# Optimization experiments

Hardware: AMD Instinct MI355X
Metric: run time of the kernel (lower is better)

Reference implementation:

```python
import jax, jax.numpy as jnp
import numpy as np

N, E, G = 50000, 800000, 200
F_IN, C, HEADS = 16, 64, 4
HID = C * HEADS  # 256


def setup_inputs() -> dict:
    key = jax.random.key(0)
    ks = jax.random.split(key, 30)
    rn = lambda k, s, sc=0.1: jax.random.normal(k, s, jnp.float32) * sc
    inp = {
        'x': jax.random.normal(ks[0], (N, F_IN), jnp.float32),
        'edge_index': jax.random.randint(ks[1], (2, E), 0, N, jnp.int32),
        'batch': jnp.sort(jax.random.randint(ks[2], (N,), 0, G, jnp.int32)),
        'Wl1': rn(ks[3], (F_IN, HID)), 'Wr1': rn(ks[4], (F_IN, HID)),
        'att1': rn(ks[5], (HEADS, C)), 'b1': rn(ks[6], (HID,)),
        'g1': jnp.ones((HID,), jnp.float32), 'be1': jnp.zeros((HID,), jnp.float32),
        'Wl2': rn(ks[7], (HID, HID)), 'Wr2': rn(ks[8], (HID, HID)),
        'att2': rn(ks[9], (HEADS, C)), 'b2': rn(ks[10], (HID,)),
        'g2': jnp.ones((HID,), jnp.float32), 'be2': jnp.zeros((HID,), jnp.float32),
        # GATv2 layer 3: 256 -> 64, 1 head, mean (concat=False)
        'Wl3': rn(ks[11], (HID, C)), 'Wr3': rn(ks[12], (HID, C)),
        'att3': rn(ks[13], (1, C)), 'b3': rn(ks[14], (C,)),
        'g3': jnp.ones((C,), jnp.float32), 'be3': jnp.zeros((C,), jnp.float32),
        # classifier MLP: 128 -> 64 -> 1
        'Wc1': rn(ks[15], (2 * C, C)), 'bc1': rn(ks[16], (C,)),
        'Wc2': rn(ks[17], (C, 1)), 'bc2': rn(ks[18], (1,)),
    }
    return inp


def _gatv2(x, src, dst, Wl, Wr, att, b, heads, c, concat):
    n = x.shape[0]
    xl = (x @ Wl).reshape(n, heads, c)
    xr = (x @ Wr).reshape(n, heads, c)
    s = jax.nn.leaky_relu(xl[src] + xr[dst], 0.2)       # [E', H, C]
    e = jnp.einsum('ehc,hc->eh', s, att)                 # [E', H]
    m = jax.ops.segment_max(e, dst, num_segments=n)
    p = jnp.exp(e - m[dst])
    denom = jax.ops.segment_sum(p, dst, num_segments=n)
    alpha = p / (denom[dst] + 1e-16)
    out = jax.ops.segment_sum(alpha[:, :, None] * xl[src], dst, num_segments=n)
    out = out.reshape(n, heads * c) if concat else out.mean(axis=1)
    return out + b


def _bn(x, g, b):
    mu = x.mean(0)
    v = x.var(0)
    return (x - mu) * jax.lax.rsqrt(v + 1e-5) * g + b


def reference(x, edge_index, batch,
              Wl1, Wr1, att1, b1, g1, be1,
              Wl2, Wr2, att2, b2, g2, be2,
              Wl3, Wr3, att3, b3, g3, be3,
              Wc1, bc1, Wc2, bc2):
    n = x.shape[0]
    loop = jnp.arange(n, dtype=edge_index.dtype)
    src = jnp.concatenate([edge_index[0], loop])  # PyG add_self_loops=True
    dst = jnp.concatenate([edge_index[1], loop])

    h = _gatv2(x, src, dst, Wl1, Wr1, att1, b1, HEADS, C, True)
    h = jax.nn.elu(_bn(h, g1, be1))  # dropout disabled (eval)
    h = _gatv2(h, src, dst, Wl2, Wr2, att2, b2, HEADS, C, True)
    h = jax.nn.elu(_bn(h, g2, be2))
    h = _gatv2(h, src, dst, Wl3, Wr3, att3, b3, 1, C, False)
    h = _bn(h, g3, be3)

    cnt = jax.ops.segment_sum(jnp.ones((n, 1), h.dtype), batch, num_segments=G)
    mean_pool = jax.ops.segment_sum(h, batch, num_segments=G) / jnp.maximum(cnt, 1.0)
    max_pool = jax.ops.segment_max(h, batch, num_segments=G)
    pooled = jnp.concatenate([mean_pool, max_pool], axis=1)  # [G, 128]

    out = jax.nn.relu(pooled @ Wc1 + bc1)
    out = out @ Wc2 + bc2  # [G, 1]
    return out
```

## Files before the change

### kernel.cpp

```cpp
#include <hip/hip_runtime.h>
#include <math.h>

#define N_NODES 50000
#define N_EDGES 800000
#define ET (N_EDGES + N_NODES)
#define N_GRAPHS 200
#define F_INN 16
#define C_DIM 64
#define N_HEADS 4
#define HIDD 256
#define SCAN_BLOCKS ((N_NODES + 255) / 256)

typedef __attribute__((ext_vector_type(8))) short short8;
typedef __attribute__((ext_vector_type(4))) float f32x4;
typedef __attribute__((ext_vector_type(2))) float f32x2;

__device__ __forceinline__ float bf2f(ushort u) {
  return __uint_as_float(((unsigned)u) << 16);
}
__device__ __forceinline__ ushort f2bf(float f) {
  unsigned u = __float_as_uint(f);
  u += 0x7fff + ((u >> 16) & 1);
  return (ushort)(u >> 16);
}

__device__ __forceinline__ f32x2 emax2(f32x2 a, f32x2 b) {
#if __has_builtin(__builtin_elementwise_max)
  return __builtin_elementwise_max(a, b);
#else
  f32x2 r;
  r.x = fmaxf(a.x, b.x);
  r.y = fmaxf(a.y, b.y);
  return r;
#endif
}

template<int K, int M>
__global__ __launch_bounds__(256) void gemm_dual(
    const float* __restrict__ A, const float* __restrict__ Bl,
    const float* __restrict__ Br, ushort* __restrict__ Clb,
    float* __restrict__ Cr, int nrows)
{
  __shared__ __align__(16) float As[16][64];
  __shared__ __align__(16) float Bls[16][64];
  __shared__ __align__(16) float Brs[16][64];
  int tid = threadIdx.x;
  int row0 = blockIdx.x * 64;
  int col0 = blockIdx.y * 64;
  int tr = (tid >> 4) << 2;
  int tc = (tid & 15) << 2;
  float accL[4][4] = {{0.f}}, accR[4][4] = {{0.f}};
  int arow = tid >> 2, ak = (tid & 3) << 2;
  int brow = tid >> 4, bcol = (tid & 15) << 2;
  for (int k0 = 0; k0 < K; k0 += 16) {
    float4 av = make_float4(0.f, 0.f, 0.f, 0.f);
    int gr = row0 + arow;
    if (gr < nrows) av = *(const float4*)&A[(size_t)gr * K + k0 + ak];
    As[ak + 0][arow] = av.x;
    As[ak + 1][arow] = av.y;
    As[ak + 2][arow] = av.z;
    As[ak + 3][arow] = av.w;
    *(float4*)&Bls[brow][bcol] = *(const float4*)&Bl[(size_t)(k0 + brow) * M + col0 + bcol];
    *(float4*)&Brs[brow][bcol] = *(const float4*)&Br[(size_t)(k0 + brow) * M + col0 + bcol];
    __syncthreads();
    #pragma unroll
    for (int k = 0; k < 16; ++k) {
      float4 a = *(const float4*)&As[k][tr];
      float4 bl = *(const float4*)&Bls[k][tc];
      float4 br = *(const float4*)&Brs[k][tc];
      float aa[4] = {a.x, a.y, a.z, a.w};
      float lb[4] = {bl.x, bl.y, bl.z, bl.w};
      float rb[4] = {br.x, br.y, br.z, br.w};
      #pragma unroll
      for (int ii = 0; ii < 4; ++ii)
        #pragma unroll
        for (int jj = 0; jj < 4; ++jj) {
          accL[ii][jj] = fmaf(aa[ii], lb[jj], accL[ii][jj]);
          accR[ii][jj] = fmaf(aa[ii], rb[jj], accR[ii][jj]);
        }
    }
    __syncthreads();
  }
  #pragma unroll
  for (int ii = 0; ii < 4; ++ii) {
    int gr = row0 + tr + ii;
    if (gr < nrows) {
      *(ushort4*)&Clb[(size_t)gr * M + col0 + tc] =
          make_ushort4(f2bf(accL[ii][0]), f2bf(accL[ii][1]),
                       f2bf(accL[ii][2]), f2bf(accL[ii][3]));
      *(float4*)&Cr[(size_t)gr * M + col0 + tc] =
          make_float4(accR[ii][0], accR[ii][1], accR[ii][2], accR[ii][3]);
    }
  }
}

__device__ __forceinline__ void split_bf16(float a, ushort& hi, ushort& lo) {
  unsigned u = __float_as_uint(a);
  hi = (ushort)(u >> 16);
  float ah = __uint_as_float(u & 0xffff0000u);
  float r = a - ah;
  lo = (ushort)(__float_as_uint(r) >> 16);
}

template<int K, int N>
__global__ void convertB(const float* __restrict__ W, ushort* __restrict__ BTmat) {
  int idx = blockIdx.x * blockDim.x + threadIdx.x;
  if (idx >= K * N) return;
  int k = idx / N, n = idx - k * N;
  ushort hi, lo;
  split_bf16(W[idx], hi, lo);
  size_t dst = ((size_t)(k >> 3) * N + n) * 8 + (k & 7);
  BTmat[dst] = hi;
  BTmat[(size_t)(K / 8) * N * 8 + dst] = lo;
}

template<int N>
__global__ __launch_bounds__(N * 2) void gemm_fused(
    const float* __restrict__ H, const float* __restrict__ gsum,
    const float* __restrict__ gsumsq, const float* __restrict__ g,
    const float* __restrict__ be, const ushort* __restrict__ BT,
    ushort* __restrict__ Clb, float* __restrict__ Cr)
{
  constexpr int THREADS = N * 2;
  constexpr int PLANE = 32 * N * 8;
  __shared__ float SCs[256], SHs[256];
  __shared__ ushort Ah_s[64 * 256];
  __shared__ ushort Al_s[64 * 256];
  const int tid = threadIdx.x;
  const int brow0 = blockIdx.x * 64;

  const float invn = 1.0f / (float)N_NODES;
  for (int c = tid; c < 256; c += THREADS) {
    float mu = gsum[c] * invn;
    float var = gsumsq[c] * invn - mu * mu;
    float sc = g[c] * rsqrtf(var + 1e-5f);
    SCs[c] = sc;
    SHs[c] = be[c] - mu * sc;
  }
  __syncthreads();

  for (int gid = tid; gid < 2048; gid += THREADS) {
    int r = gid >> 5;
    int ch0 = (gid & 31) * 8;
    int grow = min(brow0 + r, N_NODES - 1);
    float4 v0 = *(const float4*)&H[(size_t)grow * 256 + ch0];
    float4 v1 = *(const float4*)&H[(size_t)grow * 256 + ch0 + 4];
    float4 sc0 = *(const float4*)&SCs[ch0];
    float4 sc1 = *(const float4*)&SCs[ch0 + 4];
    float4 sh0 = *(const float4*)&SHs[ch0];
    float4 sh1 = *(const float4*)&SHs[ch0 + 4];
    float vv[8] = {v0.x, v0.y, v0.z, v0.w, v1.x, v1.y, v1.z, v1.w};
    float scv[8] = {sc0.x, sc0.y, sc0.z, sc0.w, sc1.x, sc1.y, sc1.z, sc1.w};
    float shv[8] = {sh0.x, sh0.y, sh0.z, sh0.w, sh1.x, sh1.y, sh1.z, sh1.w};
    short8 hi8, lo8;
    #pragma unroll
    for (int j = 0; j < 8; ++j) {
      float t = fmaf(vv[j], scv[j], shv[j]);
      float e = t > 0.f ? t : __expf(t) - 1.f;
      ushort h, l;
      split_bf16(e, h, l);
      hi8[j] = (short)h;
      lo8[j] = (short)l;
    }
    int off = r * 512 + ((ch0 * 2) ^ ((r & 7) << 4));
    *(short8*)((char*)Ah_s + off) = hi8;
    *(short8*)((char*)Al_s + off) = lo8;
  }
  __syncthreads();

  const int wave = tid >> 6, lane = tid & 63;
  const int cn = lane & 15, kgrp = lane >> 4;
  const int combc = wave * 64;
  const bool isR = combc >= N;
  const ushort* Bh = BT + (isR ? 2 * PLANE : 0);
  const ushort* Bl_ = Bh + PLANE;
  const int cb = combc & (N - 1);
  f32x4 acc[4][4];
  #pragma unroll
  for (int rt = 0; rt < 4; ++rt)
    #pragma unroll
    for (int ct = 0; ct < 4; ++ct) acc[rt][ct] = (f32x4)(0.f);

  #pragma unroll 2
  for (int k0 = 0; k0 < 256; k0 += 32) {
    short8 ah[4], al[4];
    #pragma unroll
    for (int rt = 0; rt < 4; ++rt) {
      int row = rt * 16 + cn;
      int off = row * 512 + (((k0 * 2) + kgrp * 16) ^ ((row & 7) << 4));
      ah[rt] = *(const short8*)((const char*)Ah_s + off);
      al[rt] = *(const short8*)((const char*)Al_s + off);
    }
    const size_t bbase = (size_t)((k0 >> 3) + kgrp) * (N * 8);
    #pragma unroll
    for (int ct = 0; ct < 4; ++ct) {
      const size_t bo = bbase + (size_t)(cb + ct * 16 + cn) * 8;
      short8 bh = *(const short8*)&Bh[bo];
      short8 bl = *(const short8*)&Bl_[bo];
      #pragma unroll
      for (int rt = 0; rt < 4; ++rt) {
        acc[rt][ct] = __builtin_amdgcn_mfma_f32_16x16x32_bf16(ah[rt], bh, acc[rt][ct], 0, 0, 0);
        acc[rt][ct] = __builtin_amdgcn_mfma_f32_16x16x32_bf16(ah[rt], bl, acc[rt][ct], 0, 0, 0);
        acc[rt][ct] = __builtin_amdgcn_mfma_f32_16x16x32_bf16(al[rt], bh, acc[rt][ct], 0, 0, 0);
      }
    }
  }

  #pragma unroll
  for (int ct = 0; ct < 4; ++ct) {
    int cc = cb + ct * 16 + cn;
    #pragma unroll
    for (int rt = 0; rt < 4; ++rt) {
      int crow0 = brow0 + rt * 16 + kgrp * 4;
      #pragma unroll
      for (int j = 0; j < 4; ++j) {
        int rr = crow0 + j;
        if (rr < N_NODES) {
          if (!isR) Clb[(size_t)rr * N + cc] = f2bf(acc[rt][ct][j]);
          else      Cr[(size_t)rr * N + cc] = acc[rt][ct][j];
        }
      }
    }
  }
}

__global__ void hist_kernel(const int* __restrict__ dsts, int* __restrict__ curs) {
  int i = blockIdx.x * blockDim.x + threadIdx.x;
  if (i >= ET) return;
  int d = (i < N_EDGES) ? dsts[i] : i - N_EDGES;
  atomicAdd(&curs[d], 1);
}

__global__ __launch_bounds__(256) void scan_part(
    const int* __restrict__ curs, int* __restrict__ rows, int* __restrict__ bsum)
{
  __shared__ int tmp[256];
  int t = threadIdx.x;
  int i = blockIdx.x * 256 + t;
  int v = (i < N_NODES) ? curs[i] : 0;
  tmp[t] = v;
  __syncthreads();
  #pragma unroll
  for (int off = 1; off < 256; off <<= 1) {
    int u = (t >= off) ? tmp[t - off] : 0;
    __syncthreads();
    tmp[t] += u;
    __syncthreads();
  }
  if (i < N_NODES) rows[i] = tmp[t] - v;
  if (t == 255) bsum[blockIdx.x] = tmp[255];
}

__global__ __launch_bounds__(256) void scan_bsums(
    const int* __restrict__ bsum, int* __restrict__ boff)
{
  __shared__ int tmp[256];
  int t = threadIdx.x;
  int v = (t < SCAN_BLOCKS) ? bsum[t] : 0;
  tmp[t] = v;
  __syncthreads();
  #pragma unroll
  for (int off = 1; off < 256; off <<= 1) {
    int u = (t >= off) ? tmp[t - off] : 0;
    __syncthreads();
    tmp[t] += u;
    __syncthreads();
  }
  if (t < SCAN_BLOCKS) boff[t] = tmp[t] - v;
}

__global__ __launch_bounds__(256) void scan_apply(
    int* __restrict__ rows, const int* __restrict__ boff, int* __restrict__ curs)
{
  int i = blockIdx.x * 256 + threadIdx.x;
  if (i < N_NODES) {
    int r = rows[i] + boff[blockIdx.x];
    rows[i] = r;
    curs[i] = r;
  }
  if (i == 0) rows[N_NODES] = ET;
}

__global__ void scatter_kernel(const int* __restrict__ srcs, const int* __restrict__ dsts,
                               int* __restrict__ curs, int* __restrict__ esrc) {
  int i = blockIdx.x * blockDim.x + threadIdx.x;
  if (i >= ET) return;
  int s, d;
  if (i < N_EDGES) { s = srcs[i]; d = dsts[i]; } else { s = d = i - N_EDGES; }
  int pos = atomicAdd(&curs[d], 1);
  esrc[pos] = s;
}

template<int HEADS_, int D_>
__global__ __launch_bounds__(256) void flash_csr(
    const ushort* __restrict__ xl, const float* __restrict__ xr,
    const float* __restrict__ att, const int* __restrict__ rows,
    const int* __restrict__ esrc, float* __restrict__ out)
{
  int d = blockIdx.x * 4 + (threadIdx.x >> 6);
  if (d >= N_NODES) return;
  int lane = threadIdx.x & 63;
  int beg = rows[d], end = rows[d + 1];
  if constexpr (D_ == 256) {
    float4 xrvf = *(const float4*)&xr[(size_t)d * 256 + lane * 4];
    float4 wf = *(const float4*)&att[lane * 4];
    f32x2 xr01 = {xrvf.x, xrvf.y}, xr23 = {xrvf.z, xrvf.w};
    f32x2 w01 = {wf.x, wf.y}, w23 = {wf.z, wf.w};
    float m = -INFINITY, s = 0.f;
    f32x2 a01 = {0.f, 0.f}, a23 = {0.f, 0.f};

    auto loadb = [&](int src, f32x2& ba, f32x2& bb) {
      ushort4 u = *(const ushort4*)&xl[(size_t)src * 256 + lane * 4];
      ba = f32x2{bf2f(u.x), bf2f(u.y)};
      bb = f32x2{bf2f(u.z), bf2f(u.w)};
    };
    auto scoreP = [&](f32x2 ba, f32x2 bb) -> float {
      f32x2 v01 = ba + xr01, v23 = bb + xr23;
      v01 = emax2(v01, v01 * 0.2f);
      v23 = emax2(v23, v23 * 0.2f);
      f32x2 dd = v01 * w01 + v23 * w23;
      return dd.x + dd.y;
    };
    auto one_edge = [&](int src) {
      f32x2 ba, bb;
      loadb(src, ba, bb);
      float e = scoreP(ba, bb);
      e += __shfl_xor(e, 1);
      e += __shfl_xor(e, 2);
      e += __shfl_xor(e, 4);
      e += __shfl_xor(e, 8);
      float mn = fmaxf(m, e);
      float f = __expf(m - mn);
      float pe = __expf(e - mn);
      s = s * f + pe;
      a01 = a01 * f + ba * pe;
      a23 = a23 * f + bb * pe;
      m = mn;
    };

    int p = beg;
    int head = min(end, (beg + 3) & ~3);
    for (; p < head; ++p) one_edge(esrc[p]);
    for (; p + 4 <= end; p += 4) {
      int4 sv = *(const int4*)&esrc[p];
      f32x2 b1a, b1b, b2a, b2b, b3a, b3b, b4a, b4b;
      loadb(sv.x, b1a, b1b);
      loadb(sv.y, b2a, b2b);
      loadb(sv.z, b3a, b3b);
      loadb(sv.w, b4a, b4b);
      float e1 = scoreP(b1a, b1b);
      float e2 = scoreP(b2a, b2b);
      float e3 = scoreP(b3a, b3b);
      float e4 = scoreP(b4a, b4b);
      e1 += __shfl_xor(e1, 1); e2 += __shfl_xor(e2, 1);
      e3 += __shfl_xor(e3, 1); e4 += __shfl_xor(e4, 1);
      e1 += __shfl_xor(e1, 2); e2 += __shfl_xor(e2, 2);
      e3 += __shfl_xor(e3, 2); e4 += __shfl_xor(e4, 2);
      e1 += __shfl_xor(e1, 4); e2 += __shfl_xor(e2, 4);
      e3 += __shfl_xor(e3, 4); e4 += __shfl_xor(e4, 4);
      e1 += __shfl_xor(e1, 8); e2 += __shfl_xor(e2, 8);
      e3 += __shfl_xor(e3, 8); e4 += __shfl_xor(e4, 8);
      float mn = fmaxf(fmaxf(m, fmaxf(e1, e2)), fmaxf(e3, e4));
      float f = __expf(m - mn);
      float p1 = __expf(e1 - mn);
      float p2 = __expf(e2 - mn);
      float p3 = __expf(e3 - mn);
      float p4 = __expf(e4 - mn);
      s = s * f + ((p1 + p2) + (p3 + p4));
      f32x2 t01 = b1a * p1 + b2a * p2;
      f32x2 u01 = b3a * p3 + b4a * p4;
      a01 = a01 * f + (t01 + u01);
      f32x2 t23 = b1b * p1 + b2b * p2;
      f32x2 u23 = b3b * p3 + b4b * p4;
      a23 = a23 * f + (t23 + u23);
      m = mn;
    }
    for (; p < end; ++p) one_edge(esrc[p]);

    float inv = 1.f / (s + 1e-16f);
    *(float4*)&out[(size_t)d * 256 + lane * 4] =
        make_float4(a01.x * inv, a01.y * inv, a23.x * inv, a23.y * inv);
  } else {
    float xrv = xr[(size_t)d * 64 + lane];
    float w = att[lane];
    float m = -INFINITY, s = 0.f, acc = 0.f;
    int p = beg;
    for (; p + 2 <= end; p += 2) {
      int s1 = esrc[p], s2 = esrc[p + 1];
      float b1 = bf2f(xl[(size_t)s1 * 64 + lane]);
      float b2 = bf2f(xl[(size_t)s2 * 64 + lane]);
      float v1 = b1 + xrv, v2 = b2 + xrv;
      v1 = fmaxf(v1, 0.2f * v1);
      v2 = fmaxf(v2, 0.2f * v2);
      float e1 = v1 * w, e2 = v2 * w;
      e1 += __shfl_xor(e1, 1);  e2 += __shfl_xor(e2, 1);
      e1 += __shfl_xor(e1, 2);  e2 += __shfl_xor(e2, 2);
      e1 += __shfl_xor(e1, 4);  e2 += __shfl_xor(e2, 4);
      e1 += __shfl_xor(e1, 8);  e2 += __shfl_xor(e2, 8);
      e1 += __shfl_xor(e1, 16); e2 += __shfl_xor(e2, 16);
      e1 += __shfl_xor(e1, 32); e2 += __shfl_xor(e2, 32);
      float mn = fmaxf(m, fmaxf(e1, e2));
      float f = __expf(m - mn);
      float p1 = __expf(e1 - mn);
      float p2 = __expf(e2 - mn);
      s = fmaf(s, f, p1 + p2);
      acc = fmaf(acc, f, fmaf(p1, b1, p2 * b2));
      m = mn;
    }
    if (p < end) {
      int s1 = esrc[p];
      float b1 = bf2f(xl[(size_t)s1 * 64 + lane]);
      float v1 = b1 + xrv;
      v1 = fmaxf(v1, 0.2f * v1);
      float e1 = v1 * w;
      e1 += __shfl_xor(e1, 1);
      e1 += __shfl_xor(e1, 2);
      e1 += __shfl_xor(e1, 4);
      e1 += __shfl_xor(e1, 8);
      e1 += __shfl_xor(e1, 16);
      e1 += __shfl_xor(e1, 32);
      float mn = fmaxf(m, e1);
      float f = __expf(m - mn);
      float p1 = __expf(e1 - mn);
      s = fmaf(s, f, p1);
      acc = fmaf(acc, f, p1 * b1);
    }
    out[(size_t)d * 64 + lane] = acc / (s + 1e-16f);
  }
}

template<int D_, int RPB>
__global__ __launch_bounds__(256) void bn_stats(const float* __restrict__ h,
    float* __restrict__ gsum, float* __restrict__ gsumsq, int nrows)
{
  constexpr int RG = 256 / D_;
  int c = threadIdx.x % D_;
  int rg = threadIdx.x / D_;
  int r0 = blockIdx.x * RPB;
  float s = 0.f, sq = 0.f;
  int rend = min(r0 + RPB, nrows);
  for (int r = r0 + rg; r < rend; r += RG) {
    float v = h[(size_t)r * D_ + c];
    s += v;
    sq = fmaf(v, v, sq);
  }
  atomicAdd(&gsum[c], s);
  atomicAdd(&gsumsq[c], sq);
}

__global__ __launch_bounds__(256) void pool_mlp(
    const float* __restrict__ h3, const int* __restrict__ batch,
    const float* __restrict__ gsum, const float* __restrict__ gsumsq,
    const float* __restrict__ g3, const float* __restrict__ be3,
    const float* __restrict__ Wc1, const float* __restrict__ bc1,
    const float* __restrict__ Wc2, const float* __restrict__ bc2,
    float* __restrict__ outp)
{
  int g = blockIdx.x;
  int t = threadIdx.x;
  int lane = t & 63, w = t >> 6;
  int lo, hi;
  {
    int a = 0, b = N_NODES;
    while (a < b) { int mid = (a + b) >> 1; if (batch[mid] < g) a = mid + 1; else b = mid; }
    lo = a;
    b = N_NODES;
    while (a < b) { int mid = (a + b) >> 1; if (batch[mid] < g + 1) a = mid + 1; else b = mid; }
    hi = a;
  }
  const float invn = 1.0f / (float)N_NODES;
  float mu = gsum[lane] * invn;
  float var = gsumsq[lane] * invn - mu * mu;
  float scl = g3[lane] * rsqrtf(var + 1e-5f);
  float shf = be3[lane] - mu * scl;
  float s = 0.f, mx = -INFINITY;
  for (int r = lo + w; r < hi; r += 4) {
    float v = fmaf(h3[(size_t)r * 64 + lane], scl, shf);
    s += v;
    mx = fmaxf(mx, v);
  }
  __shared__ float ssum[4][64];
  __shared__ float smax[4][64];
  __shared__ float pooled[128];
  ssum[w][lane] = s;
  smax[w][lane] = mx;
  __syncthreads();
  if (w == 0) {
    float tot = ssum[0][lane] + ssum[1][lane] + ssum[2][lane] + ssum[3][lane];
    float m4 = fmaxf(fmaxf(smax[0][lane], smax[1][lane]),
                     fmaxf(smax[2][lane], smax[3][lane]));
    float cnt = (float)(hi - lo);
    pooled[lane] = tot / fmaxf(cnt, 1.f);
    pooled[64 + lane] = m4;
  }
  __syncthreads();
  if (w == 0) {
    float a = bc1[lane];
    #pragma unroll 8
    for (int k = 0; k < 128; ++k) a = fmaf(pooled[k], Wc1[k * 64 + lane], a);
    a = fmaxf(a, 0.f);
    float v = a * Wc2[lane];
    v += __shfl_xor(v, 1);
    v += __shfl_xor(v, 2);
    v += __shfl_xor(v, 4);
    v += __shfl_xor(v, 8);
    v += __shfl_xor(v, 16);
    v += __shfl_xor(v, 32);
    if (lane == 0) outp[g] = v + bc2[0];
  }
}

extern "C" void kernel_launch(void* const* d_in, const int* in_sizes, int n_in,
                              void* d_out, int out_size, void* d_ws, size_t ws_size,
                              hipStream_t stream)
{
  const float* x    = (const float*)d_in[0];
  const int*   ei   = (const int*)d_in[1];
  const int*   batch= (const int*)d_in[2];
  const float* Wl1  = (const float*)d_in[3];
  const float* Wr1  = (const float*)d_in[4];
  const float* att1 = (const float*)d_in[5];
  const float* g1   = (const float*)d_in[7];
  const float* be1  = (const float*)d_in[8];
  const float* Wl2  = (const float*)d_in[9];
  const float* Wr2  = (const float*)d_in[10];
  const float* att2 = (const float*)d_in[11];
  const float* g2   = (const float*)d_in[13];
  const float* be2  = (const float*)d_in[14];
  const float* Wl3  = (const float*)d_in[15];
  const float* Wr3  = (const float*)d_in[16];
  const float* att3 = (const float*)d_in[17];
  const float* g3   = (const float*)d_in[19];
  const float* be3  = (const float*)d_in[20];
  const float* Wc1  = (const float*)d_in[21];
  const float* bc1  = (const float*)d_in[22];
  const float* Wc2  = (const float*)d_in[23];
  const float* bc2  = (const float*)d_in[24];

  const int* srcs = ei;
  const int* dsts = ei + N_EDGES;

  float* ws = (float*)d_ws;
  size_t o = 0;
  ushort* XLB = (ushort*)(ws + o); o += (size_t)N_NODES * HIDD / 2;
  float* XR = ws + o;            o += (size_t)N_NODES * HIDD;
  float* Hb = ws + o;            o += (size_t)N_NODES * HIDD;
  ushort* BT2 = (ushort*)(ws + o); o += (size_t)4 * 32 * 256 * 8 / 2;
  ushort* BT3 = (ushort*)(ws + o); o += (size_t)4 * 32 * 64 * 8 / 2;
  int* ESRC = (int*)(ws + o);    o += ET;
  int* ROWS = (int*)(ws + o);    o += N_NODES + 1;
  int* CURS = (int*)(ws + o);    o += N_NODES;
  int* BSUM = (int*)(ws + o);    o += SCAN_BLOCKS;
  int* BOFF = (int*)(ws + o);    o += SCAN_BLOCKS;
  float* GS  = ws + o;           o += 256;
  float* GSQ = ws + o;           o += 256;

  const int ROW_BLOCKS = (N_NODES + 63) / 64;
  const int DST_BLOCKS = (N_NODES + 3) / 4;
  constexpr int PLANE2 = 32 * 256 * 8;
  constexpr int PLANE3 = 32 * 64 * 8;

  convertB<256, 256><<<(65536 + 255) / 256, 256, 0, stream>>>(Wl2, BT2);
  convertB<256, 256><<<(65536 + 255) / 256, 256, 0, stream>>>(Wr2, BT2 + 2 * PLANE2);
  convertB<256, 64><<<(16384 + 255) / 256, 256, 0, stream>>>(Wl3, BT3);
  convertB<256, 64><<<(16384 + 255) / 256, 256, 0, stream>>>(Wr3, BT3 + 2 * PLANE3);

  hipMemsetAsync(CURS, 0, N_NODES * 4, stream);
  hist_kernel<<<(ET + 255) / 256, 256, 0, stream>>>(dsts, CURS);
  scan_part<<<SCAN_BLOCKS, 256, 0, stream>>>(CURS, ROWS, BSUM);
  scan_bsums<<<1, 256, 0, stream>>>(BSUM, BOFF);
  scan_apply<<<SCAN_BLOCKS, 256, 0, stream>>>(ROWS, BOFF, CURS);
  scatter_kernel<<<(ET + 255) / 256, 256, 0, stream>>>(srcs, dsts, CURS, ESRC);

  gemm_dual<16, 256><<<dim3(ROW_BLOCKS, 4), 256, 0, stream>>>(
      x, Wl1, Wr1, XLB, XR, N_NODES);
  flash_csr<4, 256><<<DST_BLOCKS, 256, 0, stream>>>(XLB, XR, att1, ROWS, ESRC, Hb);
  hipMemsetAsync(GS, 0, 512 * 4, stream);
  bn_stats<256, 64><<<ROW_BLOCKS, 256, 0, stream>>>(Hb, GS, GSQ, N_NODES);

  gemm_fused<256><<<ROW_BLOCKS, 512, 0, stream>>>(
      Hb, GS, GSQ, g1, be1, BT2, XLB, XR);
  flash_csr<4, 256><<<DST_BLOCKS, 256, 0, stream>>>(XLB, XR, att2, ROWS, ESRC, Hb);
  hipMemsetAsync(GS, 0, 512 * 4, stream);
  bn_stats<256, 64><<<ROW_BLOCKS, 256, 0, stream>>>(Hb, GS, GSQ, N_NODES);

  gemm_fused<64><<<ROW_BLOCKS, 128, 0, stream>>>(
      Hb, GS, GSQ, g2, be2, BT3, XLB, XR);
  flash_csr<1, 64><<<DST_BLOCKS, 256, 0, stream>>>(XLB, XR, att3, ROWS, ESRC, Hb);
  hipMemsetAsync(GS, 0, 512 * 4, stream);
  bn_stats<64, 256><<<(N_NODES + 255) / 256, 256, 0, stream>>>(Hb, GS, GSQ, N_NODES);

  pool_mlp<<<N_GRAPHS, 256, 0, stream>>>(Hb, batch, GS, GSQ, g3, be3,
                                         Wc1, bc1, Wc2, bc2, (float*)d_out);
}
```

Measured before the change: 604.9 us.

## Pack multiple destination nodes per wavefront in GATv2 aggregation kernels

Result: faster. 577.8 us (-4.5%).

```diff
diff --git a/kernel.cpp b/kernel.cpp
--- a/kernel.cpp
+++ b/kernel.cpp
@@ -12,6 +12,7 @@
 #define SCAN_BLOCKS ((N_NODES + 255) / 256)
 
 typedef __attribute__((ext_vector_type(8))) short short8;
+typedef __attribute__((ext_vector_type(8))) ushort ushort8;
 typedef __attribute__((ext_vector_type(4))) float f32x4;
 typedef __attribute__((ext_vector_type(2))) float f32x2;
 
@@ -291,141 +292,197 @@
   esrc[pos] = s;
 }
 
-template<int HEADS_, int D_>
-__global__ __launch_bounds__(256) void flash_csr(
+__global__ __launch_bounds__(256) void flash256(
     const ushort* __restrict__ xl, const float* __restrict__ xr,
     const float* __restrict__ att, const int* __restrict__ rows,
     const int* __restrict__ esrc, float* __restrict__ out)
 {
-  int d = blockIdx.x * 4 + (threadIdx.x >> 6);
-  if (d >= N_NODES) return;
-  int lane = threadIdx.x & 63;
+  const int wave = threadIdx.x >> 6, lane = threadIdx.x & 63;
+  const int half = lane >> 5, sl = lane & 31;
+  const int d = blockIdx.x * 8 + wave * 2 + half;
+  const int ch = sl * 8;
+  float4 xa = *(const float4*)&xr[(size_t)d * 256 + ch];
+  float4 xb = *(const float4*)&xr[(size_t)d * 256 + ch + 4];
+  float4 wa = *(const float4*)&att[ch];
+  float4 wb = *(const float4*)&att[ch + 4];
+  f32x2 xr0 = {xa.x, xa.y}, xr1 = {xa.z, xa.w}, xr2 = {xb.x, xb.y}, xr3 = {xb.z, xb.w};
+  f32x2 w0 = {wa.x, wa.y}, w1 = {wa.z, wa.w}, w2 = {wb.x, wb.y}, w3 = {wb.z, wb.w};
   int beg = rows[d], end = rows[d + 1];
-  if constexpr (D_ == 256) {
-    float4 xrvf = *(const float4*)&xr[(size_t)d * 256 + lane * 4];
-    float4 wf = *(const float4*)&att[lane * 4];
-    f32x2 xr01 = {xrvf.x, xrvf.y}, xr23 = {xrvf.z, xrvf.w};
-    f32x2 w01 = {wf.x, wf.y}, w23 = {wf.z, wf.w};
-    float m = -INFINITY, s = 0.f;
-    f32x2 a01 = {0.f, 0.f}, a23 = {0.f, 0.f};
-
-    auto loadb = [&](int src, f32x2& ba, f32x2& bb) {
-      ushort4 u = *(const ushort4*)&xl[(size_t)src * 256 + lane * 4];
-      ba = f32x2{bf2f(u.x), bf2f(u.y)};
-      bb = f32x2{bf2f(u.z), bf2f(u.w)};
-    };
-    auto scoreP = [&](f32x2 ba, f32x2 bb) -> float {
-      f32x2 v01 = ba + xr01, v23 = bb + xr23;
-      v01 = emax2(v01, v01 * 0.2f);
-      v23 = emax2(v23, v23 * 0.2f);
-      f32x2 dd = v01 * w01 + v23 * w23;
-      return dd.x + dd.y;
-    };
-    auto one_edge = [&](int src) {
-      f32x2 ba, bb;
-      loadb(src, ba, bb);
-      float e = scoreP(ba, bb);
-      e += __shfl_xor(e, 1);
-      e += __shfl_xor(e, 2);
-      e += __shfl_xor(e, 4);
-      e += __shfl_xor(e, 8);
-      float mn = fmaxf(m, e);
-      float f = __expf(m - mn);
-      float pe = __expf(e - mn);
-      s = s * f + pe;
-      a01 = a01 * f + ba * pe;
-      a23 = a23 * f + bb * pe;
-      m = mn;
-    };
-
-    int p = beg;
-    int head = min(end, (beg + 3) & ~3);
-    for (; p < head; ++p) one_edge(esrc[p]);
-    for (; p + 4 <= end; p += 4) {
-      int4 sv = *(const int4*)&esrc[p];
-      f32x2 b1a, b1b, b2a, b2b, b3a, b3b, b4a, b4b;
-      loadb(sv.x, b1a, b1b);
-      loadb(sv.y, b2a, b2b);
-      loadb(sv.z, b3a, b3b);
-      loadb(sv.w, b4a, b4b);
-      float e1 = scoreP(b1a, b1b);
-      float e2 = scoreP(b2a, b2b);
-      float e3 = scoreP(b3a, b3b);
-      float e4 = scoreP(b4a, b4b);
-      e1 += __shfl_xor(e1, 1); e2 += __shfl_xor(e2, 1);
-      e3 += __shfl_xor(e3, 1); e4 += __shfl_xor(e4, 1);
-      e1 += __shfl_xor(e1, 2); e2 += __shfl_xor(e2, 2);
-      e3 += __shfl_xor(e3, 2); e4 += __shfl_xor(e4, 2);
-      e1 += __shfl_xor(e1, 4); e2 += __shfl_xor(e2, 4);
-      e3 += __shfl_xor(e3, 4); e4 += __shfl_xor(e4, 4);
-      e1 += __shfl_xor(e1, 8); e2 += __shfl_xor(e2, 8);
-      e3 += __shfl_xor(e3, 8); e4 += __shfl_xor(e4, 8);
-      float mn = fmaxf(fmaxf(m, fmaxf(e1, e2)), fmaxf(e3, e4));
-      float f = __expf(m - mn);
-      float p1 = __expf(e1 - mn);
-      float p2 = __expf(e2 - mn);
-      float p3 = __expf(e3 - mn);
-      float p4 = __expf(e4 - mn);
-      s = s * f + ((p1 + p2) + (p3 + p4));
-      f32x2 t01 = b1a * p1 + b2a * p2;
-      f32x2 u01 = b3a * p3 + b4a * p4;
-      a01 = a01 * f + (t01 + u01);
-      f32x2 t23 = b1b * p1 + b2b * p2;
-      f32x2 u23 = b3b * p3 + b4b * p4;
-      a23 = a23 * f + (t23 + u23);
-      m = mn;
-    }
-    for (; p < end; ++p) one_edge(esrc[p]);
-
+  float m = -INFINITY, s = 0.f;
+  f32x2 a0 = {0.f, 0.f}, a1 = {0.f, 0.f}, a2 = {0.f, 0.f}, a3 = {0.f, 0.f};
+
+  auto loadb = [&](int src, f32x2 b[4]) {
+    ushort8 u = *(const ushort8*)&xl[(size_t)src * 256 + ch];
+    b[0] = f32x2{bf2f(u[0]), bf2f(u[1])};
+    b[1] = f32x2{bf2f(u[2]), bf2f(u[3])};
+    b[2] = f32x2{bf2f(u[4]), bf2f(u[5])};
+    b[3] = f32x2{bf2f(u[6]), bf2f(u[7])};
+  };
+  auto scoreP = [&](const f32x2 b[4]) -> float {
+    f32x2 v0 = b[0] + xr0, v1 = b[1] + xr1, v2 = b[2] + xr2, v3 = b[3] + xr3;
+    v0 = emax2(v0, v0 * 0.2f);
+    v1 = emax2(v1, v1 * 0.2f);
+    v2 = emax2(v2, v2 * 0.2f);
+    v3 = emax2(v3, v3 * 0.2f);
+    f32x2 dd = (v0 * w0 + v1 * w1) + (v2 * w2 + v3 * w3);
+    return dd.x + dd.y;
+  };
+  auto one_edge = [&](int src) {
+    f32x2 b[4];
+    loadb(src, b);
+    float e = scoreP(b);
+    e += __shfl_xor(e, 1);
+    e += __shfl_xor(e, 2);
+    e += __shfl_xor(e, 4);
+    float mn = fmaxf(m, e);
+    float f = __expf(m - mn);
+    float pe = __expf(e - mn);
+    s = s * f + pe;
+    a0 = a0 * f + b[0] * pe;
+    a1 = a1 * f + b[1] * pe;
+    a2 = a2 * f + b[2] * pe;
+    a3 = a3 * f + b[3] * pe;
+    m = mn;
+  };
+
+  int p = beg;
+  int hd = min(end, (beg + 3) & ~3);
+  for (; p < hd; ++p) one_edge(esrc[p]);
+  for (; p + 4 <= end; p += 4) {
+    int4 sv = *(const int4*)&esrc[p];
+    f32x2 b1[4], b2[4], b3[4], b4[4];
+    loadb(sv.x, b1);
+    loadb(sv.y, b2);
+    loadb(sv.z, b3);
+    loadb(sv.w, b4);
+    float e1 = scoreP(b1);
+    float e2 = scoreP(b2);
+    float e3 = scoreP(b3);
+    float e4 = scoreP(b4);
+    e1 += __shfl_xor(e1, 1); e2 += __shfl_xor(e2, 1);
+    e3 += __shfl_xor(e3, 1); e4 += __shfl_xor(e4, 1);
+    e1 += __shfl_xor(e1, 2); e2 += __shfl_xor(e2, 2);
+    e3 += __shfl_xor(e3, 2); e4 += __shfl_xor(e4, 2);
+    e1 += __shfl_xor(e1, 4); e2 += __shfl_xor(e2, 4);
+    e3 += __shfl_xor(e3, 4); e4 += __shfl_xor(e4, 4);
+    float mn = fmaxf(fmaxf(m, fmaxf(e1, e2)), fmaxf(e3, e4));
+    float f = __expf(m - mn);
+    float p1 = __expf(e1 - mn);
+    float p2 = __expf(e2 - mn);
+    float p3 = __expf(e3 - mn);
+    float p4 = __expf(e4 - mn);
+    s = s * f + ((p1 + p2) + (p3 + p4));
+    a0 = a0 * f + ((b1[0] * p1 + b2[0] * p2) + (b3[0] * p3 + b4[0] * p4));
+    a1 = a1 * f + ((b1[1] * p1 + b2[1] * p2) + (b3[1] * p3 + b4[1] * p4));
+    a2 = a2 * f + ((b1[2] * p1 + b2[2] * p2) + (b3[2] * p3 + b4[2] * p4));
+    a3 = a3 * f + ((b1[3] * p1 + b2[3] * p2) + (b3[3] * p3 + b4[3] * p4));
+    m = mn;
+  }
+  for (; p < end; ++p) one_edge(esrc[p]);
+
+  float inv = 1.f / (s + 1e-16f);
+  *(float4*)&out[(size_t)d * 256 + ch] =
+      make_float4(a0.x * inv, a0.y * inv, a1.x * inv, a1.y * inv);
+  *(float4*)&out[(size_t)d * 256 + ch + 4] =
+      make_float4(a2.x * inv, a2.y * inv, a3.x * inv, a3.y * inv);
+}
+
+__global__ __launch_bounds__(256) void flash64(
+    const ushort* __restrict__ xl, const float* __restrict__ xr,
+    const float* __restrict__ att, const int* __restrict__ rows,
+    const int* __restrict__ esrc, float* __restrict__ out)
+{
+  const int wave = threadIdx.x >> 6, lane = threadIdx.x & 63;
+  const int di = lane >> 3, sl = lane & 7;
+  const int d = blockIdx.x * 32 + wave * 8 + di;
+  const bool valid = d < N_NODES;
+  const int dc = valid ? d : N_NODES - 1;
+  const int ch = sl * 8;
+  float4 xa = *(const float4*)&xr[(size_t)dc * 64 + ch];
+  float4 xb = *(const float4*)&xr[(size_t)dc * 64 + ch + 4];
+  float4 wa = *(const float4*)&att[ch];
+  float4 wb = *(const float4*)&att[ch + 4];
+  f32x2 xr0 = {xa.x, xa.y}, xr1 = {xa.z, xa.w}, xr2 = {xb.x, xb.y}, xr3 = {xb.z, xb.w};
+  f32x2 w0 = {wa.x, wa.y}, w1 = {wa.z, wa.w}, w2 = {wb.x, wb.y}, w3 = {wb.z, wb.w};
+  int beg = rows[dc], end = rows[dc + 1];
+  float m = -INFINITY, s = 0.f;
+  f32x2 a0 = {0.f, 0.f}, a1 = {0.f, 0.f}, a2 = {0.f, 0.f}, a3 = {0.f, 0.f};
+
+  auto loadb = [&](int src, f32x2 b[4]) {
+    ushort8 u = *(const ushort8*)&xl[(size_t)src * 64 + ch];
+    b[0] = f32x2{bf2f(u[0]), bf2f(u[1])};
+    b[1] = f32x2{bf2f(u[2]), bf2f(u[3])};
+    b[2] = f32x2{bf2f(u[4]), bf2f(u[5])};
+    b[3] = f32x2{bf2f(u[6]), bf2f(u[7])};
+  };
+  auto scoreP = [&](const f32x2 b[4]) -> float {
+    f32x2 v0 = b[0] + xr0, v1 = b[1] + xr1, v2 = b[2] + xr2, v3 = b[3] + xr3;
+    v0 = emax2(v0, v0 * 0.2f);
+    v1 = emax2(v1, v1 * 0.2f);
+    v2 = emax2(v2, v2 * 0.2f);
+    v3 = emax2(v3, v3 * 0.2f);
+    f32x2 dd = (v0 * w0 + v1 * w1) + (v2 * w2 + v3 * w3);
+    return dd.x + dd.y;
+  };
+  auto one_edge = [&](int src) {
+    f32x2 b[4];
+    loadb(src, b);
+    float e = scoreP(b);
+    e += __shfl_xor(e, 1);
+    e += __shfl_xor(e, 2);
+    e += __shfl_xor(e, 4);
+    float mn = fmaxf(m, e);
+    float f = __expf(m - mn);
+    float pe = __expf(e - mn);
+    s = s * f + pe;
+    a0 = a0 * f + b[0] * pe;
+    a1 = a1 * f + b[1] * pe;
+    a2 = a2 * f + b[2] * pe;
+    a3 = a3 * f + b[3] * pe;
+    m = mn;
+  };
+
+  int p = beg;
+  int hd = min(end, (beg + 3) & ~3);
+  for (; p < hd; ++p) one_edge(esrc[p]);
+  for (; p + 4 <= end; p += 4) {
+    int4 sv = *(const int4*)&esrc[p];
+    f32x2 b1[4], b2[4], b3[4], b4[4];
+    loadb(sv.x, b1);
+    loadb(sv.y, b2);
+    loadb(sv.z, b3);
+    loadb(sv.w, b4);
+    float e1 = scoreP(b1);
+    float e2 = scoreP(b2);
+    float e3 = scoreP(b3);
+    float e4 = scoreP(b4);
+    e1 += __shfl_xor(e1, 1); e2 += __shfl_xor(e2, 1);
+    e3 += __shfl_xor(e3, 1); e4 += __shfl_xor(e4, 1);
+    e1 += __shfl_xor(e1, 2); e2 += __shfl_xor(e2, 2);
+    e3 += __shfl_xor(e3, 2); e4 += __shfl_xor(e4, 2);
+    e1 += __shfl_xor(e1, 4); e2 += __shfl_xor(e2, 4);
+    e3 += __shfl_xor(e3, 4); e4 += __shfl_xor(e4, 4);
+    float mn = fmaxf(fmaxf(m, fmaxf(e1, e2)), fmaxf(e3, e4));
+    float f = __expf(m - mn);
+    float p1 = __expf(e1 - mn);
+    float p2 = __expf(e2 - mn);
+    float p3 = __expf(e3 - mn);
+    float p4 = __expf(e4 - mn);
+    s = s * f + ((p1 + p2) + (p3 + p4));
+    a0 = a0 * f + ((b1[0] * p1 + b2[0] * p2) + (b3[0] * p3 + b4[0] * p4));
+    a1 = a1 * f + ((b1[1] * p1 + b2[1] * p2) + (b3[1] * p3 + b4[1] * p4));
+    a2 = a2 * f + ((b1[2] * p1 + b2[2] * p2) + (b3[2] * p3 + b4[2] * p4));
+    a3 = a3 * f + ((b1[3] * p1 + b2[3] * p2) + (b3[3] * p3 + b4[3] * p4));
+    m = mn;
+  }
+  for (; p < end; ++p) one_edge(esrc[p]);
+
+  if (valid) {
     float inv = 1.f / (s + 1e-16f);
-    *(float4*)&out[(size_t)d * 256 + lane * 4] =
-        make_float4(a01.x * inv, a01.y * inv, a23.x * inv, a23.y * inv);
-  } else {
-    float xrv = xr[(size_t)d * 64 + lane];
-    float w = att[lane];
-    float m = -INFINITY, s = 0.f, acc = 0.f;
-    int p = beg;
-    for (; p + 2 <= end; p += 2) {
-      int s1 = esrc[p], s2 = esrc[p + 1];
-      float b1 = bf2f(xl[(size_t)s1 * 64 + lane]);
-      float b2 = bf2f(xl[(size_t)s2 * 64 + lane]);
-      float v1 = b1 + xrv, v2 = b2 + xrv;
-      v1 = fmaxf(v1, 0.2f * v1);
-      v2 = fmaxf(v2, 0.2f * v2);
-      float e1 = v1 * w, e2 = v2 * w;
-      e1 += __shfl_xor(e1, 1);  e2 += __shfl_xor(e2, 1);
-      e1 += __shfl_xor(e1, 2);  e2 += __shfl_xor(e2, 2);
-      e1 += __shfl_xor(e1, 4);  e2 += __shfl_xor(e2, 4);
-      e1 += __shfl_xor(e1, 8);  e2 += __shfl_xor(e2, 8);
-      e1 += __shfl_xor(e1, 16); e2 += __shfl_xor(e2, 16);
-      e1 += __shfl_xor(e1, 32); e2 += __shfl_xor(e2, 32);
-      float mn = fmaxf(m, fmaxf(e1, e2));
-      float f = __expf(m - mn);
-      float p1 = __expf(e1 - mn);
-      float p2 = __expf(e2 - mn);
-      s = fmaf(s, f, p1 + p2);
-      acc = fmaf(acc, f, fmaf(p1, b1, p2 * b2));
-      m = mn;
-    }
-    if (p < end) {
-      int s1 = esrc[p];
-      float b1 = bf2f(xl[(size_t)s1 * 64 + lane]);
-      float v1 = b1 + xrv;
-      v1 = fmaxf(v1, 0.2f * v1);
-      float e1 = v1 * w;
-      e1 += __shfl_xor(e1, 1);
-      e1 += __shfl_xor(e1, 2);
-      e1 += __shfl_xor(e1, 4);
-      e1 += __shfl_xor(e1, 8);
-      e1 += __shfl_xor(e1, 16);
-      e1 += __shfl_xor(e1, 32);
-      float mn = fmaxf(m, e1);
-      float f = __expf(m - mn);
-      float p1 = __expf(e1 - mn);
-      s = fmaf(s, f, p1);
-      acc = fmaf(acc, f, p1 * b1);
-    }
-    out[(size_t)d * 64 + lane] = acc / (s + 1e-16f);
+    *(float4*)&out[(size_t)d * 64 + ch] =
+        make_float4(a0.x * inv, a0.y * inv, a1.x * inv, a1.y * inv);
+    *(float4*)&out[(size_t)d * 64 + ch + 4] =
+        make_float4(a2.x * inv, a2.y * inv, a3.x * inv, a3.y * inv);
   }
 }
 
@@ -556,7 +613,6 @@
   float* GSQ = ws + o;           o += 256;
 
   const int ROW_BLOCKS = (N_NODES + 63) / 64;
-  const int DST_BLOCKS = (N_NODES + 3) / 4;
   constexpr int PLANE2 = 32 * 256 * 8;
   constexpr int PLANE3 = 32 * 64 * 8;
 
@@ -574,19 +630,19 @@
 
   gemm_dual<16, 256><<<dim3(ROW_BLOCKS, 4), 256, 0, stream>>>(
       x, Wl1, Wr1, XLB, XR, N_NODES);
-  flash_csr<4, 256><<<DST_BLOCKS, 256, 0, stream>>>(XLB, XR, att1, ROWS, ESRC, Hb);
+  flash256<<<N_NODES / 8, 256, 0, stream>>>(XLB, XR, att1, ROWS, ESRC, Hb);
   hipMemsetAsync(GS, 0, 512 * 4, stream);
   bn_stats<256, 64><<<ROW_BLOCKS, 256, 0, stream>>>(Hb, GS, GSQ, N_NODES);
 
   gemm_fused<256><<<ROW_BLOCKS, 512, 0, stream>>>(
       Hb, GS, GSQ, g1, be1, BT2, XLB, XR);
-  flash_csr<4, 256><<<DST_BLOCKS, 256, 0, stream>>>(XLB, XR, att2, ROWS, ESRC, Hb);
+  flash256<<<N_NODES / 8, 256, 0, stream>>>(XLB, XR, att2, ROWS, ESRC, Hb);
   hipMemsetAsync(GS, 0, 512 * 4, stream);
   bn_stats<256, 64><<<ROW_BLOCKS, 256, 0, stream>>>(Hb, GS, GSQ, N_NODES);
 
   gemm_fused<64><<<ROW_BLOCKS, 128, 0, stream>>>(
       Hb, GS, GSQ, g2, be2, BT3, XLB, XR);
-  flash_csr<1, 64><<<DST_BLOCKS, 256, 0, stream>>>(XLB, XR, att3, ROWS, ESRC, Hb);
+  flash64<<<(N_NODES + 31) / 32, 256, 0, stream>>>(XLB, XR, att3, ROWS, ESRC, Hb);
   hipMemsetAsync(GS, 0, 512 * 4, stream);
   bn_stats<64, 256><<<(N_NODES + 255) / 256, 256, 0, stream>>>(Hb, GS, GSQ, N_NODES);
 
```
